# Kernel optimization log

Measured on AMD Instinct MI355X. Metric: run time of the kernel, lower is better.

Reference implementation:

```python
import jax, jax.numpy as jnp
import numpy as np

WS = 8        # window_size -> N = 64
P = 8         # patch_size
HEADS = 3
DIM = 96
B = 2048


def _relative_positions_log(ws):
    coords = jnp.stack(jnp.meshgrid(jnp.arange(ws), jnp.arange(ws), indexing='ij'))  # [2,ws,ws]
    cf = coords.reshape(2, -1)                                   # [2, N]
    rel = cf[:, :, None] - cf[:, None, :]                        # [2, N, N]
    rel = rel.transpose(1, 2, 0).astype(jnp.float32)             # [N, N, 2]
    return jnp.sign(rel) * jnp.log1p(jnp.abs(rel))


def setup_inputs() -> dict:
    key = jax.random.key(0)
    k0, k1, k2 = jax.random.split(key, 3)
    N = WS * WS
    qkv = jax.random.normal(k0, (B, N, 3 * DIM), dtype=jnp.float32)
    w1 = jax.random.normal(k1, (2, 256), dtype=jnp.float32) * 0.02
    b1 = jnp.zeros((256,), dtype=jnp.float32)
    w2 = jax.random.normal(k2, (256, HEADS), dtype=jnp.float32) * 0.02
    b2 = jnp.zeros((HEADS,), dtype=jnp.float32)
    return {"qkv": qkv, "w1": w1, "b1": b1, "w2": w2, "b2": b2}


def reference(qkv, w1, b1, w2, b2):
    B_, N, C3 = qkv.shape
    dim = C3 // 3
    h = HEADS
    d = dim // h
    scale = d ** (-0.5)

    qkv = qkv.reshape(B_, N, 3, h, d).transpose(2, 0, 3, 1, 4)   # [3,B,h,N,d]
    q, k, v = qkv[0] * scale, qkv[1], qkv[2]

    c = N // (P * P)
    def to_patch(x):  # [B,h,N,d] -> [B,h,c,d,P,P]
        return x.reshape(B_, h, c, P, P, d).transpose(0, 1, 2, 5, 3, 4)

    q_fft = jnp.fft.rfft2(to_patch(q))
    k_fft = jnp.fft.rfft2(to_patch(k))
    out = jnp.fft.irfft2(q_fft * k_fft, s=(P, P))                # [B,h,c,d,P,P]
    out = out.transpose(0, 1, 2, 4, 5, 3).reshape(B_, h, N, d)   # back to [B,h,N,d]

    rp = _relative_positions_log(WS)                             # [N,N,2]
    bias = jax.nn.relu(rp @ w1 + b1) @ w2 + b2                   # [N,N,h]
    bias = bias.transpose(2, 0, 1)                               # [h,N,N]

    attn = jnp.einsum('bhnd,bhmd->bhnm', out, v) + bias[None]
    attn = jax.nn.softmax(attn, axis=-1)
    x = jnp.einsum('bhnm,bhmd->bhnd', attn, v)
    return x.transpose(0, 2, 1, 3).reshape(B_, N, dim)
```

## Files before the change

### kernel.cpp

```cpp
#include <hip/hip_runtime.h>

#define B_TOT 2048
#define NHEAD 3

typedef __attribute__((ext_vector_type(8))) short short8v;
typedef __attribute__((ext_vector_type(4))) float f32x4;
typedef __attribute__((ext_vector_type(2))) __fp16 f16x2;

#define LOG2E 1.4426950408889634f

static __device__ __forceinline__ unsigned short f2bf(float x) {
    unsigned u = __builtin_bit_cast(unsigned, x);
    u += 0x7FFFu + ((u >> 16) & 1u);
    return (unsigned short)(u >> 16);
}
static __device__ __forceinline__ float bf2f(unsigned short s) {
    unsigned u = ((unsigned)s) << 16;
    return __builtin_bit_cast(float, u);
}
static __device__ __forceinline__ float exp2_fast(float x) {
    float r; asm("v_exp_f32 %0, %1" : "=v"(r) : "v"(x)); return r;
}

__global__ __launch_bounds__(256) void bias_kernel(const float* __restrict__ w1,
                                                   const float* __restrict__ b1,
                                                   const float* __restrict__ w2,
                                                   const float* __restrict__ b2,
                                                   float* __restrict__ bias2) {
    int t = blockIdx.x * 256 + threadIdx.x;
    int h = t >> 12;
    int lane = (t >> 6) & 63;
    int pair = t & 63;
    int g = lane >> 4, c = lane & 15;
    int mt = pair >> 4, nt = (pair >> 2) & 3, r = pair & 3;
    int n = 16 * mt + 4 * g + r;
    int m = 16 * nt + c;

    float d0 = (float)((n >> 3) - (m >> 3));
    float d1 = (float)((n & 7) - (m & 7));
    float r0 = (d0 > 0.f ? 1.f : (d0 < 0.f ? -1.f : 0.f)) * log1pf(fabsf(d0));
    float r1 = (d1 > 0.f ? 1.f : (d1 < 0.f ? -1.f : 0.f)) * log1pf(fabsf(d1));
    float a = 0.f;
    for (int j = 0; j < 256; j++) {
        float hd = fmaf(r0, w1[j], fmaf(r1, w1[256 + j], b1[j]));
        hd = fmaxf(hd, 0.f);
        a = fmaf(hd, w2[j * 3 + h], a);
    }
    bias2[((h * 16 + mt * 4 + nt) * 64 + lane) * 4 + r] = (a + b2[h]) * LOG2E;
}

__global__ __launch_bounds__(256, 3) void attn_kernel(const float* __restrict__ qkv,
                                                      const float* __restrict__ bias2,
                                                      float* __restrict__ out) {
    __shared__ float smem[4][64 * 36];

    const int t = threadIdx.x;
    const int w = t >> 6;
    const int lane = t & 63;
    const int h = blockIdx.x % 3;
    const int b = (blockIdx.x / 3) * 4 + w;

    float* Qs = smem[w];
    const float* base = qkv + (size_t)b * (64 * 288) + h * 32;
    const float QS = 0.17677669529663687f * LOG2E;

    {
        const int nr = lane >> 3, d0 = (lane & 7) * 4;
        #pragma unroll
        for (int s = 0; s < 8; s++) {
            int n = 8 * s + nr;
            float4 q4 = *(const float4*)(base + n * 288 + d0);
            q4.x *= QS; q4.y *= QS; q4.z *= QS; q4.w *= QS;
            *(float4*)(Qs + n * 36 + d0) = q4;
        }
    }

    const int dd = lane & 31, H2 = lane >> 5;
    f16x2 krp[64];
    #pragma unroll
    for (int t8 = 0; t8 < 8; t8++) {
        const int rb = ((t8 + 4 * H2) & 7) * 8;
        float k8[8];
        #pragma unroll
        for (int tx = 0; tx < 8; tx++)
            k8[tx] = base[(rb + tx) * 288 + 96 + dd];
        #pragma unroll
        for (int i = 0; i < 8; i++)
            krp[t8 * 8 + i] = __builtin_amdgcn_cvt_pkrtz(k8[i], k8[(i - 1) & 7]);
    }

    asm volatile("s_waitcnt lgkmcnt(0)" ::: "memory");

    float acc[4][8];
    #pragma unroll
    for (int yi = 0; yi < 4; yi++)
        #pragma unroll
        for (int x = 0; x < 8; x++) acc[yi][x] = 0.f;

    #pragma unroll
    for (int u = 0; u < 8; u++) {
        f16x2 q2[4];
        #pragma unroll
        for (int j = 0; j < 4; j++) {
            float qa = Qs[(u * 8 + 2 * j) * 36 + dd];
            float qb = Qs[(u * 8 + 2 * j + 1) * 36 + dd];
            q2[j] = __builtin_amdgcn_cvt_pkrtz(qa, qb);
        }
        #pragma unroll
        for (int yi = 0; yi < 4; yi++) {
            const int s = (yi - u) & 7;
            #pragma unroll
            for (int x = 0; x < 8; x++) {
                #pragma unroll
                for (int j = 0; j < 4; j++)
                    acc[yi][x] = __builtin_amdgcn_fdot2(
                        q2[j], krp[s * 8 + ((x - 2 * j) & 7)], acc[yi][x], false);
            }
        }
    }

    #pragma unroll
    for (int yi = 0; yi < 4; yi++) {
        const int n = (4 * H2 + yi) * 8;
        #pragma unroll
        for (int x = 0; x < 8; x++)
            Qs[(n + x) * 36 + dd] = acc[yi][x];
    }
    asm volatile("s_waitcnt lgkmcnt(0)" ::: "memory");

    const int g = lane >> 4, c = lane & 15;

    short8v Oh[4], Ol[4];
    #pragma unroll
    for (int mt = 0; mt < 4; mt++) {
        const float* rp = Qs + (16 * mt + c) * 36 + 8 * g;
        float4 x0 = *(const float4*)rp;
        float4 x1 = *(const float4*)(rp + 4);
        float xs[8] = {x0.x, x0.y, x0.z, x0.w, x1.x, x1.y, x1.z, x1.w};
        #pragma unroll
        for (int j = 0; j < 8; j++) {
            unsigned short hb = f2bf(xs[j]);
            Oh[mt][j] = (short)hb;
            Ol[mt][j] = (short)f2bf(xs[j] - bf2f(hb));
        }
    }

    short8v Vh[4], Vl[4];
    #pragma unroll
    for (int nt = 0; nt < 4; nt++) {
        const float* vp = base + (16 * nt + c) * 288 + 192 + 8 * g;
        float4 x0 = *(const float4*)vp;
        float4 x1 = *(const float4*)(vp + 4);
        float xs[8] = {x0.x, x0.y, x0.z, x0.w, x1.x, x1.y, x1.z, x1.w};
        #pragma unroll
        for (int j = 0; j < 8; j++) {
            unsigned short hb = f2bf(xs[j]);
            Vh[nt][j] = (short)hb;
            Vl[nt][j] = (short)f2bf(xs[j] - bf2f(hb));
        }
    }

    const float* bb = bias2 + (size_t)h * 16 * 256 + lane * 4;
    f32x4 S[4][4];
    __builtin_amdgcn_s_setprio(1);
    #pragma unroll
    for (int mt = 0; mt < 4; mt++)
        #pragma unroll
        for (int nt = 0; nt < 4; nt++) {
            f32x4 a = __builtin_bit_cast(f32x4, *(const float4*)(bb + (mt * 4 + nt) * 256));
            a = __builtin_amdgcn_mfma_f32_16x16x32_bf16(Oh[mt], Vh[nt], a, 0, 0, 0);
            a = __builtin_amdgcn_mfma_f32_16x16x32_bf16(Oh[mt], Vl[nt], a, 0, 0, 0);
            a = __builtin_amdgcn_mfma_f32_16x16x32_bf16(Ol[mt], Vh[nt], a, 0, 0, 0);
            S[mt][nt] = a;
        }
    __builtin_amdgcn_s_setprio(0);

    float vb[2][2][8];
    #pragma unroll
    for (int kt = 0; kt < 2; kt++)
        #pragma unroll
        for (int dt = 0; dt < 2; dt++)
            #pragma unroll
            for (int j = 0; j < 8; j++)
                vb[kt][dt][j] = base[(32 * kt + 8 * g + j) * 288 + 192 + 16 * dt + c];

    #pragma unroll
    for (int mt = 0; mt < 4; mt++) {
        #pragma unroll
        for (int r = 0; r < 4; r++) {
            float m0 = fmaxf(fmaxf(S[mt][0][r], S[mt][1][r]), fmaxf(S[mt][2][r], S[mt][3][r]));
            m0 = fmaxf(m0, __shfl_xor(m0, 1, 64));
            m0 = fmaxf(m0, __shfl_xor(m0, 2, 64));
            m0 = fmaxf(m0, __shfl_xor(m0, 4, 64));
            m0 = fmaxf(m0, __shfl_xor(m0, 8, 64));
            #pragma unroll
            for (int nt = 0; nt < 4; nt++)
                S[mt][nt][r] = exp2_fast(S[mt][nt][r] - m0);
        }
    }

    unsigned short* Ps = (unsigned short*)Qs;
    #pragma unroll
    for (int mt = 0; mt < 4; mt++)
        #pragma unroll
        for (int nt = 0; nt < 4; nt++)
            #pragma unroll
            for (int r = 0; r < 4; r++)
                Ps[(16 * mt + 4 * g + r) * 72 + 16 * nt + c] = f2bf(S[mt][nt][r]);
    asm volatile("s_waitcnt lgkmcnt(0)" ::: "memory");

    short8v Pf[4][2];
    #pragma unroll
    for (int mt = 0; mt < 4; mt++)
        #pragma unroll
        for (int kt = 0; kt < 2; kt++)
            Pf[mt][kt] = *(const short8v*)(Ps + (16 * mt + c) * 72 + 32 * kt + 8 * g);

    short8v Vp[2][2];
    #pragma unroll
    for (int kt = 0; kt < 2; kt++)
        #pragma unroll
        for (int dt = 0; dt < 2; dt++)
            #pragma unroll
            for (int j = 0; j < 8; j++)
                Vp[kt][dt][j] = (short)f2bf(vb[kt][dt][j]);

    short8v ones;
    #pragma unroll
    for (int j = 0; j < 8; j++) ones[j] = (short)0x3F80;
    f32x4 inv4[4];
    __builtin_amdgcn_s_setprio(1);
    #pragma unroll
    for (int mt = 0; mt < 4; mt++) {
        f32x4 sa = {0.f, 0.f, 0.f, 0.f};
        sa = __builtin_amdgcn_mfma_f32_16x16x32_bf16(Pf[mt][0], ones, sa, 0, 0, 0);
        sa = __builtin_amdgcn_mfma_f32_16x16x32_bf16(Pf[mt][1], ones, sa, 0, 0, 0);
        #pragma unroll
        for (int r = 0; r < 4; r++) inv4[mt][r] = 1.f / sa[r];
    }

    f32x4 X[4][2];
    #pragma unroll
    for (int mt = 0; mt < 4; mt++)
        #pragma unroll
        for (int dt = 0; dt < 2; dt++) {
            f32x4 a = {0.f, 0.f, 0.f, 0.f};
            a = __builtin_amdgcn_mfma_f32_16x16x32_bf16(Pf[mt][0], Vp[0][dt], a, 0, 0, 0);
            a = __builtin_amdgcn_mfma_f32_16x16x32_bf16(Pf[mt][1], Vp[1][dt], a, 0, 0, 0);
            X[mt][dt] = a;
        }
    __builtin_amdgcn_s_setprio(0);

    float* op = out + (size_t)b * (64 * 96) + h * 32;
    #pragma unroll
    for (int mt = 0; mt < 4; mt++)
        #pragma unroll
        for (int dt = 0; dt < 2; dt++)
            #pragma unroll
            for (int r = 0; r < 4; r++)
                op[(16 * mt + 4 * g + r) * 96 + 16 * dt + c] = X[mt][dt][r] * inv4[mt][r];
}

extern "C" void kernel_launch(void* const* d_in, const int* in_sizes, int n_in,
                              void* d_out, int out_size, void* d_ws, size_t ws_size,
                              hipStream_t stream) {
    const float* qkv = (const float*)d_in[0];
    const float* w1  = (const float*)d_in[1];
    const float* b1  = (const float*)d_in[2];
    const float* w2  = (const float*)d_in[3];
    const float* b2  = (const float*)d_in[4];
    float* out = (float*)d_out;
    float* bias2 = (float*)d_ws;

    bias_kernel<<<48, 256, 0, stream>>>(w1, b1, w2, b2, bias2);
    attn_kernel<<<(B_TOT / 4) * NHEAD, 256, 0, stream>>>(qkv, bias2, out);
}
```

Measured before the change: 64.95 us.

## Read Q directly from global, hoist V loads earlier, split bias MLP across lanes

The Q staging through shared memory is dropped; each lane now reads scaled Q values straight from global memory inside the FFT-convolution loop. V fragment and vb loads are moved before the MFMA phase so their latency overlaps with the conversion work, at the cost of more live registers. The bias kernel splits each 256-term reduction across 4 lanes and combines them with shuffles, launching 4x more blocks to shorten its serial loop. The risks are register pressure at occupancy 3 and repeated uncoalesced global reads of Q.

```diff
diff --git a/kernel.cpp b/kernel.cpp
--- a/kernel.cpp
+++ b/kernel.cpp
@@ -27,7 +27,8 @@
                                                    const float* __restrict__ w2,
                                                    const float* __restrict__ b2,
                                                    float* __restrict__ bias2) {
-    int t = blockIdx.x * 256 + threadIdx.x;
+    int gtid = blockIdx.x * 256 + threadIdx.x;
+    int t = gtid >> 2, sub = gtid & 3;
     int h = t >> 12;
     int lane = (t >> 6) & 63;
     int pair = t & 63;
@@ -41,12 +42,16 @@
     float r0 = (d0 > 0.f ? 1.f : (d0 < 0.f ? -1.f : 0.f)) * log1pf(fabsf(d0));
     float r1 = (d1 > 0.f ? 1.f : (d1 < 0.f ? -1.f : 0.f)) * log1pf(fabsf(d1));
     float a = 0.f;
-    for (int j = 0; j < 256; j++) {
+    for (int i = 0; i < 64; i++) {
+        int j = 4 * i + sub;
         float hd = fmaf(r0, w1[j], fmaf(r1, w1[256 + j], b1[j]));
         hd = fmaxf(hd, 0.f);
         a = fmaf(hd, w2[j * 3 + h], a);
     }
-    bias2[((h * 16 + mt * 4 + nt) * 64 + lane) * 4 + r] = (a + b2[h]) * LOG2E;
+    a += __shfl_xor(a, 1, 64);
+    a += __shfl_xor(a, 2, 64);
+    if (sub == 0)
+        bias2[((h * 16 + mt * 4 + nt) * 64 + lane) * 4 + r] = (a + b2[h]) * LOG2E;
 }
 
 __global__ __launch_bounds__(256, 3) void attn_kernel(const float* __restrict__ qkv,
@@ -63,19 +68,9 @@
     float* Qs = smem[w];
     const float* base = qkv + (size_t)b * (64 * 288) + h * 32;
     const float QS = 0.17677669529663687f * LOG2E;
-
-    {
-        const int nr = lane >> 3, d0 = (lane & 7) * 4;
-        #pragma unroll
-        for (int s = 0; s < 8; s++) {
-            int n = 8 * s + nr;
-            float4 q4 = *(const float4*)(base + n * 288 + d0);
-            q4.x *= QS; q4.y *= QS; q4.z *= QS; q4.w *= QS;
-            *(float4*)(Qs + n * 36 + d0) = q4;
-        }
-    }
-
     const int dd = lane & 31, H2 = lane >> 5;
+    const int g = lane >> 4, c = lane & 15;
+
     f16x2 krp[64];
     #pragma unroll
     for (int t8 = 0; t8 < 8; t8++) {
@@ -89,8 +84,6 @@
             krp[t8 * 8 + i] = __builtin_amdgcn_cvt_pkrtz(k8[i], k8[(i - 1) & 7]);
     }
 
-    asm volatile("s_waitcnt lgkmcnt(0)" ::: "memory");
-
     float acc[4][8];
     #pragma unroll
     for (int yi = 0; yi < 4; yi++)
@@ -102,8 +95,8 @@
         f16x2 q2[4];
         #pragma unroll
         for (int j = 0; j < 4; j++) {
-            float qa = Qs[(u * 8 + 2 * j) * 36 + dd];
-            float qb = Qs[(u * 8 + 2 * j + 1) * 36 + dd];
+            float qa = base[(u * 8 + 2 * j) * 288 + dd] * QS;
+            float qb = base[(u * 8 + 2 * j + 1) * 288 + dd] * QS;
             q2[j] = __builtin_amdgcn_cvt_pkrtz(qa, qb);
         }
         #pragma unroll
@@ -126,9 +119,24 @@
         for (int x = 0; x < 8; x++)
             Qs[(n + x) * 36 + dd] = acc[yi][x];
     }
+
+    float4 vr0[4], vr1[4];
+    #pragma unroll
+    for (int nt = 0; nt < 4; nt++) {
+        const float* vp = base + (16 * nt + c) * 288 + 192 + 8 * g;
+        vr0[nt] = *(const float4*)vp;
+        vr1[nt] = *(const float4*)(vp + 4);
+    }
+    float vb[2][2][8];
+    #pragma unroll
+    for (int kt = 0; kt < 2; kt++)
+        #pragma unroll
+        for (int dt = 0; dt < 2; dt++)
+            #pragma unroll
+            for (int j = 0; j < 8; j++)
+                vb[kt][dt][j] = base[(32 * kt + 8 * g + j) * 288 + 192 + 16 * dt + c];
+
     asm volatile("s_waitcnt lgkmcnt(0)" ::: "memory");
-
-    const int g = lane >> 4, c = lane & 15;
 
     short8v Oh[4], Ol[4];
     #pragma unroll
@@ -148,10 +156,8 @@
     short8v Vh[4], Vl[4];
     #pragma unroll
     for (int nt = 0; nt < 4; nt++) {
-        const float* vp = base + (16 * nt + c) * 288 + 192 + 8 * g;
-        float4 x0 = *(const float4*)vp;
-        float4 x1 = *(const float4*)(vp + 4);
-        float xs[8] = {x0.x, x0.y, x0.z, x0.w, x1.x, x1.y, x1.z, x1.w};
+        float xs[8] = {vr0[nt].x, vr0[nt].y, vr0[nt].z, vr0[nt].w,
+                       vr1[nt].x, vr1[nt].y, vr1[nt].z, vr1[nt].w};
         #pragma unroll
         for (int j = 0; j < 8; j++) {
             unsigned short hb = f2bf(xs[j]);
@@ -174,15 +180,6 @@
             S[mt][nt] = a;
         }
     __builtin_amdgcn_s_setprio(0);
-
-    float vb[2][2][8];
-    #pragma unroll
-    for (int kt = 0; kt < 2; kt++)
-        #pragma unroll
-        for (int dt = 0; dt < 2; dt++)
-            #pragma unroll
-            for (int j = 0; j < 8; j++)
-                vb[kt][dt][j] = base[(32 * kt + 8 * g + j) * 288 + 192 + 16 * dt + c];
 
     #pragma unroll
     for (int mt = 0; mt < 4; mt++) {
@@ -272,6 +269,6 @@
     float* out = (float*)d_out;
     float* bias2 = (float*)d_ws;
 
-    bias_kernel<<<48, 256, 0, stream>>>(w1, b1, w2, b2, bias2);
+    bias_kernel<<<192, 256, 0, stream>>>(w1, b1, w2, b2, bias2);
     attn_kernel<<<(B_TOT / 4) * NHEAD, 256, 0, stream>>>(qkv, bias2, out);
 }
```

Result: no change. 65.98 us (+1.6%).

## Process two (batch, head) units per wave and split bias reduction across lanes

Applied to the files above, without the earlier changes.

Each wave now handles two (batch, head) work units, interleaving their FFT-circulant fdot2 loops for more instruction-level parallelism, then runs the softmax/PV stage for each in turn. Shared memory doubles, launch bounds drop to 2 blocks per CU and the grid halves. Separately, the bias MLP reduction is split across 4 lanes with shuffle reduction and 4x more blocks, to shorten its serial 256-iteration loop. The doubled register footprint (two krp arrays of 64 packed halves) risks spills or lower occupancy.

```diff
diff --git a/kernel.cpp b/kernel.cpp
--- a/kernel.cpp
+++ b/kernel.cpp
@@ -27,7 +27,8 @@
                                                    const float* __restrict__ w2,
                                                    const float* __restrict__ b2,
                                                    float* __restrict__ bias2) {
-    int t = blockIdx.x * 256 + threadIdx.x;
+    int gtid = blockIdx.x * 256 + threadIdx.x;
+    int t = gtid >> 2, sub = gtid & 3;
     int h = t >> 12;
     int lane = (t >> 6) & 63;
     int pair = t & 63;
@@ -41,70 +42,87 @@
     float r0 = (d0 > 0.f ? 1.f : (d0 < 0.f ? -1.f : 0.f)) * log1pf(fabsf(d0));
     float r1 = (d1 > 0.f ? 1.f : (d1 < 0.f ? -1.f : 0.f)) * log1pf(fabsf(d1));
     float a = 0.f;
-    for (int j = 0; j < 256; j++) {
+    for (int i = 0; i < 64; i++) {
+        int j = 4 * i + sub;
         float hd = fmaf(r0, w1[j], fmaf(r1, w1[256 + j], b1[j]));
         hd = fmaxf(hd, 0.f);
         a = fmaf(hd, w2[j * 3 + h], a);
     }
-    bias2[((h * 16 + mt * 4 + nt) * 64 + lane) * 4 + r] = (a + b2[h]) * LOG2E;
-}
-
-__global__ __launch_bounds__(256, 3) void attn_kernel(const float* __restrict__ qkv,
+    a += __shfl_xor(a, 1, 64);
+    a += __shfl_xor(a, 2, 64);
+    if (sub == 0)
+        bias2[((h * 16 + mt * 4 + nt) * 64 + lane) * 4 + r] = (a + b2[h]) * LOG2E;
+}
+
+__global__ __launch_bounds__(256, 2) void attn_kernel(const float* __restrict__ qkv,
                                                       const float* __restrict__ bias2,
                                                       float* __restrict__ out) {
-    __shared__ float smem[4][64 * 36];
+    __shared__ float smem[8][64 * 36];
 
     const int t = threadIdx.x;
     const int w = t >> 6;
     const int lane = t & 63;
-    const int h = blockIdx.x % 3;
-    const int b = (blockIdx.x / 3) * 4 + w;
-
-    float* Qs = smem[w];
-    const float* base = qkv + (size_t)b * (64 * 288) + h * 32;
+    const int u0 = (blockIdx.x * 4 + w) * 2;
+    const int u1 = u0 + 1;
+    const int b0 = u0 / 3, h0 = u0 % 3;
+    const int b1 = u1 / 3, h1 = u1 % 3;
+
+    float* QsA = smem[w * 2];
+    float* QsB = smem[w * 2 + 1];
+    const float* baseA = qkv + (size_t)b0 * (64 * 288) + h0 * 32;
+    const float* baseB = qkv + (size_t)b1 * (64 * 288) + h1 * 32;
     const float QS = 0.17677669529663687f * LOG2E;
+    const int dd = lane & 31, H2 = lane >> 5;
+    const int g = lane >> 4, c = lane & 15;
 
     {
         const int nr = lane >> 3, d0 = (lane & 7) * 4;
         #pragma unroll
         for (int s = 0; s < 8; s++) {
             int n = 8 * s + nr;
-            float4 q4 = *(const float4*)(base + n * 288 + d0);
-            q4.x *= QS; q4.y *= QS; q4.z *= QS; q4.w *= QS;
-            *(float4*)(Qs + n * 36 + d0) = q4;
-        }
-    }
-
-    const int dd = lane & 31, H2 = lane >> 5;
-    f16x2 krp[64];
+            float4 qa = *(const float4*)(baseA + n * 288 + d0);
+            float4 qb = *(const float4*)(baseB + n * 288 + d0);
+            qa.x *= QS; qa.y *= QS; qa.z *= QS; qa.w *= QS;
+            qb.x *= QS; qb.y *= QS; qb.z *= QS; qb.w *= QS;
+            *(float4*)(QsA + n * 36 + d0) = qa;
+            *(float4*)(QsB + n * 36 + d0) = qb;
+        }
+    }
+
+    f16x2 krpA[64], krpB[64];
     #pragma unroll
     for (int t8 = 0; t8 < 8; t8++) {
         const int rb = ((t8 + 4 * H2) & 7) * 8;
-        float k8[8];
-        #pragma unroll
-        for (int tx = 0; tx < 8; tx++)
-            k8[tx] = base[(rb + tx) * 288 + 96 + dd];
-        #pragma unroll
-        for (int i = 0; i < 8; i++)
-            krp[t8 * 8 + i] = __builtin_amdgcn_cvt_pkrtz(k8[i], k8[(i - 1) & 7]);
+        float kA[8], kB[8];
+        #pragma unroll
+        for (int tx = 0; tx < 8; tx++) {
+            kA[tx] = baseA[(rb + tx) * 288 + 96 + dd];
+            kB[tx] = baseB[(rb + tx) * 288 + 96 + dd];
+        }
+        #pragma unroll
+        for (int i = 0; i < 8; i++) {
+            krpA[t8 * 8 + i] = __builtin_amdgcn_cvt_pkrtz(kA[i], kA[(i - 1) & 7]);
+            krpB[t8 * 8 + i] = __builtin_amdgcn_cvt_pkrtz(kB[i], kB[(i - 1) & 7]);
+        }
     }
 
     asm volatile("s_waitcnt lgkmcnt(0)" ::: "memory");
 
-    float acc[4][8];
+    float accA[4][8], accB[4][8];
     #pragma unroll
     for (int yi = 0; yi < 4; yi++)
         #pragma unroll
-        for (int x = 0; x < 8; x++) acc[yi][x] = 0.f;
+        for (int x = 0; x < 8; x++) { accA[yi][x] = 0.f; accB[yi][x] = 0.f; }
 
     #pragma unroll
     for (int u = 0; u < 8; u++) {
-        f16x2 q2[4];
+        f16x2 q2A[4], q2B[4];
         #pragma unroll
         for (int j = 0; j < 4; j++) {
-            float qa = Qs[(u * 8 + 2 * j) * 36 + dd];
-            float qb = Qs[(u * 8 + 2 * j + 1) * 36 + dd];
-            q2[j] = __builtin_amdgcn_cvt_pkrtz(qa, qb);
+            q2A[j] = __builtin_amdgcn_cvt_pkrtz(QsA[(u * 8 + 2 * j) * 36 + dd],
+                                                QsA[(u * 8 + 2 * j + 1) * 36 + dd]);
+            q2B[j] = __builtin_amdgcn_cvt_pkrtz(QsB[(u * 8 + 2 * j) * 36 + dd],
+                                                QsB[(u * 8 + 2 * j + 1) * 36 + dd]);
         }
         #pragma unroll
         for (int yi = 0; yi < 4; yi++) {
@@ -112,9 +130,12 @@
             #pragma unroll
             for (int x = 0; x < 8; x++) {
                 #pragma unroll
-                for (int j = 0; j < 4; j++)
-                    acc[yi][x] = __builtin_amdgcn_fdot2(
-                        q2[j], krp[s * 8 + ((x - 2 * j) & 7)], acc[yi][x], false);
+                for (int j = 0; j < 4; j++) {
+                    accA[yi][x] = __builtin_amdgcn_fdot2(
+                        q2A[j], krpA[s * 8 + ((x - 2 * j) & 7)], accA[yi][x], false);
+                    accB[yi][x] = __builtin_amdgcn_fdot2(
+                        q2B[j], krpB[s * 8 + ((x - 2 * j) & 7)], accB[yi][x], false);
+                }
             }
         }
     }
@@ -123,142 +144,148 @@
     for (int yi = 0; yi < 4; yi++) {
         const int n = (4 * H2 + yi) * 8;
         #pragma unroll
-        for (int x = 0; x < 8; x++)
-            Qs[(n + x) * 36 + dd] = acc[yi][x];
+        for (int x = 0; x < 8; x++) {
+            QsA[(n + x) * 36 + dd] = accA[yi][x];
+            QsB[(n + x) * 36 + dd] = accB[yi][x];
+        }
     }
     asm volatile("s_waitcnt lgkmcnt(0)" ::: "memory");
 
-    const int g = lane >> 4, c = lane & 15;
-
-    short8v Oh[4], Ol[4];
-    #pragma unroll
-    for (int mt = 0; mt < 4; mt++) {
-        const float* rp = Qs + (16 * mt + c) * 36 + 8 * g;
-        float4 x0 = *(const float4*)rp;
-        float4 x1 = *(const float4*)(rp + 4);
-        float xs[8] = {x0.x, x0.y, x0.z, x0.w, x1.x, x1.y, x1.z, x1.w};
-        #pragma unroll
-        for (int j = 0; j < 8; j++) {
-            unsigned short hb = f2bf(xs[j]);
-            Oh[mt][j] = (short)hb;
-            Ol[mt][j] = (short)f2bf(xs[j] - bf2f(hb));
-        }
-    }
-
-    short8v Vh[4], Vl[4];
-    #pragma unroll
-    for (int nt = 0; nt < 4; nt++) {
-        const float* vp = base + (16 * nt + c) * 288 + 192 + 8 * g;
-        float4 x0 = *(const float4*)vp;
-        float4 x1 = *(const float4*)(vp + 4);
-        float xs[8] = {x0.x, x0.y, x0.z, x0.w, x1.x, x1.y, x1.z, x1.w};
-        #pragma unroll
-        for (int j = 0; j < 8; j++) {
-            unsigned short hb = f2bf(xs[j]);
-            Vh[nt][j] = (short)hb;
-            Vl[nt][j] = (short)f2bf(xs[j] - bf2f(hb));
-        }
-    }
-
-    const float* bb = bias2 + (size_t)h * 16 * 256 + lane * 4;
-    f32x4 S[4][4];
-    __builtin_amdgcn_s_setprio(1);
-    #pragma unroll
-    for (int mt = 0; mt < 4; mt++)
+    auto back_half = [&](const float* base, float* Qs, int h, int b) {
+        short8v Oh[4], Ol[4];
+        #pragma unroll
+        for (int mt = 0; mt < 4; mt++) {
+            const float* rp = Qs + (16 * mt + c) * 36 + 8 * g;
+            float4 x0 = *(const float4*)rp;
+            float4 x1 = *(const float4*)(rp + 4);
+            float xs[8] = {x0.x, x0.y, x0.z, x0.w, x1.x, x1.y, x1.z, x1.w};
+            #pragma unroll
+            for (int j = 0; j < 8; j++) {
+                unsigned short hb = f2bf(xs[j]);
+                Oh[mt][j] = (short)hb;
+                Ol[mt][j] = (short)f2bf(xs[j] - bf2f(hb));
+            }
+        }
+
+        short8v Vh[4], Vl[4];
         #pragma unroll
         for (int nt = 0; nt < 4; nt++) {
-            f32x4 a = __builtin_bit_cast(f32x4, *(const float4*)(bb + (mt * 4 + nt) * 256));
-            a = __builtin_amdgcn_mfma_f32_16x16x32_bf16(Oh[mt], Vh[nt], a, 0, 0, 0);
-            a = __builtin_amdgcn_mfma_f32_16x16x32_bf16(Oh[mt], Vl[nt], a, 0, 0, 0);
-            a = __builtin_amdgcn_mfma_f32_16x16x32_bf16(Ol[mt], Vh[nt], a, 0, 0, 0);
-            S[mt][nt] = a;
-        }
-    __builtin_amdgcn_s_setprio(0);
-
-    float vb[2][2][8];
-    #pragma unroll
-    for (int kt = 0; kt < 2; kt++)
-        #pragma unroll
-        for (int dt = 0; dt < 2; dt++)
-            #pragma unroll
-            for (int j = 0; j < 8; j++)
-                vb[kt][dt][j] = base[(32 * kt + 8 * g + j) * 288 + 192 + 16 * dt + c];
-
-    #pragma unroll
-    for (int mt = 0; mt < 4; mt++) {
-        #pragma unroll
-        for (int r = 0; r < 4; r++) {
-            float m0 = fmaxf(fmaxf(S[mt][0][r], S[mt][1][r]), fmaxf(S[mt][2][r], S[mt][3][r]));
-            m0 = fmaxf(m0, __shfl_xor(m0, 1, 64));
-            m0 = fmaxf(m0, __shfl_xor(m0, 2, 64));
-            m0 = fmaxf(m0, __shfl_xor(m0, 4, 64));
-            m0 = fmaxf(m0, __shfl_xor(m0, 8, 64));
+            const float* vp = base + (16 * nt + c) * 288 + 192 + 8 * g;
+            float4 x0 = *(const float4*)vp;
+            float4 x1 = *(const float4*)(vp + 4);
+            float xs[8] = {x0.x, x0.y, x0.z, x0.w, x1.x, x1.y, x1.z, x1.w};
+            #pragma unroll
+            for (int j = 0; j < 8; j++) {
+                unsigned short hb = f2bf(xs[j]);
+                Vh[nt][j] = (short)hb;
+                Vl[nt][j] = (short)f2bf(xs[j] - bf2f(hb));
+            }
+        }
+
+        const float* bb = bias2 + (size_t)h * 16 * 256 + lane * 4;
+        f32x4 S[4][4];
+        __builtin_amdgcn_s_setprio(1);
+        #pragma unroll
+        for (int mt = 0; mt < 4; mt++)
+            #pragma unroll
+            for (int nt = 0; nt < 4; nt++) {
+                f32x4 a = __builtin_bit_cast(f32x4, *(const float4*)(bb + (mt * 4 + nt) * 256));
+                a = __builtin_amdgcn_mfma_f32_16x16x32_bf16(Oh[mt], Vh[nt], a, 0, 0, 0);
+                a = __builtin_amdgcn_mfma_f32_16x16x32_bf16(Oh[mt], Vl[nt], a, 0, 0, 0);
+                a = __builtin_amdgcn_mfma_f32_16x16x32_bf16(Ol[mt], Vh[nt], a, 0, 0, 0);
+                S[mt][nt] = a;
+            }
+        __builtin_amdgcn_s_setprio(0);
+
+        float vb[2][2][8];
+        #pragma unroll
+        for (int kt = 0; kt < 2; kt++)
+            #pragma unroll
+            for (int dt = 0; dt < 2; dt++)
+                #pragma unroll
+                for (int j = 0; j < 8; j++)
+                    vb[kt][dt][j] = base[(32 * kt + 8 * g + j) * 288 + 192 + 16 * dt + c];
+
+        #pragma unroll
+        for (int mt = 0; mt < 4; mt++) {
+            #pragma unroll
+            for (int r = 0; r < 4; r++) {
+                float m0 = fmaxf(fmaxf(S[mt][0][r], S[mt][1][r]),
+                                 fmaxf(S[mt][2][r], S[mt][3][r]));
+                m0 = fmaxf(m0, __shfl_xor(m0, 1, 64));
+                m0 = fmaxf(m0, __shfl_xor(m0, 2, 64));
+                m0 = fmaxf(m0, __shfl_xor(m0, 4, 64));
+                m0 = fmaxf(m0, __shfl_xor(m0, 8, 64));
+                #pragma unroll
+                for (int nt = 0; nt < 4; nt++)
+                    S[mt][nt][r] = exp2_fast(S[mt][nt][r] - m0);
+            }
+        }
+
+        unsigned short* Ps = (unsigned short*)Qs;
+        #pragma unroll
+        for (int mt = 0; mt < 4; mt++)
             #pragma unroll
             for (int nt = 0; nt < 4; nt++)
-                S[mt][nt][r] = exp2_fast(S[mt][nt][r] - m0);
-        }
-    }
-
-    unsigned short* Ps = (unsigned short*)Qs;
-    #pragma unroll
-    for (int mt = 0; mt < 4; mt++)
-        #pragma unroll
-        for (int nt = 0; nt < 4; nt++)
-            #pragma unroll
-            for (int r = 0; r < 4; r++)
-                Ps[(16 * mt + 4 * g + r) * 72 + 16 * nt + c] = f2bf(S[mt][nt][r]);
-    asm volatile("s_waitcnt lgkmcnt(0)" ::: "memory");
-
-    short8v Pf[4][2];
-    #pragma unroll
-    for (int mt = 0; mt < 4; mt++)
+                #pragma unroll
+                for (int r = 0; r < 4; r++)
+                    Ps[(16 * mt + 4 * g + r) * 72 + 16 * nt + c] = f2bf(S[mt][nt][r]);
+        asm volatile("s_waitcnt lgkmcnt(0)" ::: "memory");
+
+        short8v Pf[4][2];
+        #pragma unroll
+        for (int mt = 0; mt < 4; mt++)
+            #pragma unroll
+            for (int kt = 0; kt < 2; kt++)
+                Pf[mt][kt] = *(const short8v*)(Ps + (16 * mt + c) * 72 + 32 * kt + 8 * g);
+
+        short8v Vp[2][2];
         #pragma unroll
         for (int kt = 0; kt < 2; kt++)
-            Pf[mt][kt] = *(const short8v*)(Ps + (16 * mt + c) * 72 + 32 * kt + 8 * g);
-
-    short8v Vp[2][2];
-    #pragma unroll
-    for (int kt = 0; kt < 2; kt++)
-        #pragma unroll
-        for (int dt = 0; dt < 2; dt++)
-            #pragma unroll
-            for (int j = 0; j < 8; j++)
-                Vp[kt][dt][j] = (short)f2bf(vb[kt][dt][j]);
-
-    short8v ones;
-    #pragma unroll
-    for (int j = 0; j < 8; j++) ones[j] = (short)0x3F80;
-    f32x4 inv4[4];
-    __builtin_amdgcn_s_setprio(1);
-    #pragma unroll
-    for (int mt = 0; mt < 4; mt++) {
-        f32x4 sa = {0.f, 0.f, 0.f, 0.f};
-        sa = __builtin_amdgcn_mfma_f32_16x16x32_bf16(Pf[mt][0], ones, sa, 0, 0, 0);
-        sa = __builtin_amdgcn_mfma_f32_16x16x32_bf16(Pf[mt][1], ones, sa, 0, 0, 0);
-        #pragma unroll
-        for (int r = 0; r < 4; r++) inv4[mt][r] = 1.f / sa[r];
-    }
-
-    f32x4 X[4][2];
-    #pragma unroll
-    for (int mt = 0; mt < 4; mt++)
-        #pragma unroll
-        for (int dt = 0; dt < 2; dt++) {
-            f32x4 a = {0.f, 0.f, 0.f, 0.f};
-            a = __builtin_amdgcn_mfma_f32_16x16x32_bf16(Pf[mt][0], Vp[0][dt], a, 0, 0, 0);
-            a = __builtin_amdgcn_mfma_f32_16x16x32_bf16(Pf[mt][1], Vp[1][dt], a, 0, 0, 0);
-            X[mt][dt] = a;
-        }
-    __builtin_amdgcn_s_setprio(0);
-
-    float* op = out + (size_t)b * (64 * 96) + h * 32;
-    #pragma unroll
-    for (int mt = 0; mt < 4; mt++)
-        #pragma unroll
-        for (int dt = 0; dt < 2; dt++)
-            #pragma unroll
-            for (int r = 0; r < 4; r++)
-                op[(16 * mt + 4 * g + r) * 96 + 16 * dt + c] = X[mt][dt][r] * inv4[mt][r];
+            #pragma unroll
+            for (int dt = 0; dt < 2; dt++)
+                #pragma unroll
+                for (int j = 0; j < 8; j++)
+                    Vp[kt][dt][j] = (short)f2bf(vb[kt][dt][j]);
+
+        short8v ones;
+        #pragma unroll
+        for (int j = 0; j < 8; j++) ones[j] = (short)0x3F80;
+        f32x4 inv4[4];
+        __builtin_amdgcn_s_setprio(1);
+        #pragma unroll
+        for (int mt = 0; mt < 4; mt++) {
+            f32x4 sa = {0.f, 0.f, 0.f, 0.f};
+            sa = __builtin_amdgcn_mfma_f32_16x16x32_bf16(Pf[mt][0], ones, sa, 0, 0, 0);
+            sa = __builtin_amdgcn_mfma_f32_16x16x32_bf16(Pf[mt][1], ones, sa, 0, 0, 0);
+            #pragma unroll
+            for (int r = 0; r < 4; r++) inv4[mt][r] = 1.f / sa[r];
+        }
+
+        f32x4 X[4][2];
+        #pragma unroll
+        for (int mt = 0; mt < 4; mt++)
+            #pragma unroll
+            for (int dt = 0; dt < 2; dt++) {
+                f32x4 a = {0.f, 0.f, 0.f, 0.f};
+                a = __builtin_amdgcn_mfma_f32_16x16x32_bf16(Pf[mt][0], Vp[0][dt], a, 0, 0, 0);
+                a = __builtin_amdgcn_mfma_f32_16x16x32_bf16(Pf[mt][1], Vp[1][dt], a, 0, 0, 0);
+                X[mt][dt] = a;
+            }
+        __builtin_amdgcn_s_setprio(0);
+
+        float* op = out + (size_t)b * (64 * 96) + h * 32;
+        #pragma unroll
+        for (int mt = 0; mt < 4; mt++)
+            #pragma unroll
+            for (int dt = 0; dt < 2; dt++)
+                #pragma unroll
+                for (int r = 0; r < 4; r++)
+                    op[(16 * mt + 4 * g + r) * 96 + 16 * dt + c] = X[mt][dt][r] * inv4[mt][r];
+    };
+
+    back_half(baseA, QsA, h0, b0);
+    back_half(baseB, QsB, h1, b1);
 }
 
 extern "C" void kernel_launch(void* const* d_in, const int* in_sizes, int n_in,
@@ -272,6 +299,6 @@
     float* out = (float*)d_out;
     float* bias2 = (float*)d_ws;
 
-    bias_kernel<<<48, 256, 0, stream>>>(w1, b1, w2, b2, bias2);
-    attn_kernel<<<(B_TOT / 4) * NHEAD, 256, 0, stream>>>(qkv, bias2, out);
-}
+    bias_kernel<<<192, 256, 0, stream>>>(w1, b1, w2, b2, bias2);
+    attn_kernel<<<(B_TOT * NHEAD) / 8, 256, 0, stream>>>(qkv, bias2, out);
+}
```

After: 77.03 us. 18.6% more time.

## Stage K via global_load_lds, prefetch Q early, split bias reduction across lanes

Applied to the files above, without the earlier changes.

K tiles are now loaded straight into LDS with global_load_lds in a coalesced pattern and read back per column, replacing strided scalar global loads. Q loads are issued up front into registers so they overlap with the K loads, and are scaled and stored to LDS afterwards. The bias kernel splits its 256-term reduction across 4 lanes with shuffle reductions and launches four times as many blocks. The attention kernel's launch bounds drop the minimum blocks per CU from 3 to 2, which allows more registers per thread but may lower occupancy.

```diff
diff --git a/kernel.cpp b/kernel.cpp
--- a/kernel.cpp
+++ b/kernel.cpp
@@ -6,6 +6,9 @@
 typedef __attribute__((ext_vector_type(8))) short short8v;
 typedef __attribute__((ext_vector_type(4))) float f32x4;
 typedef __attribute__((ext_vector_type(2))) __fp16 f16x2;
+
+typedef __attribute__((address_space(1))) const void* gas_ptr;
+typedef __attribute__((address_space(3))) void* las_ptr;
 
 #define LOG2E 1.4426950408889634f
 
@@ -27,7 +30,8 @@
                                                    const float* __restrict__ w2,
                                                    const float* __restrict__ b2,
                                                    float* __restrict__ bias2) {
-    int t = blockIdx.x * 256 + threadIdx.x;
+    int gtid = blockIdx.x * 256 + threadIdx.x;
+    int t = gtid >> 2, sub = gtid & 3;
     int h = t >> 12;
     int lane = (t >> 6) & 63;
     int pair = t & 63;
@@ -41,15 +45,19 @@
     float r0 = (d0 > 0.f ? 1.f : (d0 < 0.f ? -1.f : 0.f)) * log1pf(fabsf(d0));
     float r1 = (d1 > 0.f ? 1.f : (d1 < 0.f ? -1.f : 0.f)) * log1pf(fabsf(d1));
     float a = 0.f;
-    for (int j = 0; j < 256; j++) {
+    for (int i = 0; i < 64; i++) {
+        int j = 4 * i + sub;
         float hd = fmaf(r0, w1[j], fmaf(r1, w1[256 + j], b1[j]));
         hd = fmaxf(hd, 0.f);
         a = fmaf(hd, w2[j * 3 + h], a);
     }
-    bias2[((h * 16 + mt * 4 + nt) * 64 + lane) * 4 + r] = (a + b2[h]) * LOG2E;
-}
-
-__global__ __launch_bounds__(256, 3) void attn_kernel(const float* __restrict__ qkv,
+    a += __shfl_xor(a, 1, 64);
+    a += __shfl_xor(a, 2, 64);
+    if (sub == 0)
+        bias2[((h * 16 + mt * 4 + nt) * 64 + lane) * 4 + r] = (a + b2[h]) * LOG2E;
+}
+
+__global__ __launch_bounds__(256, 2) void attn_kernel(const float* __restrict__ qkv,
                                                       const float* __restrict__ bias2,
                                                       float* __restrict__ out) {
     __shared__ float smem[4][64 * 36];
@@ -63,19 +71,24 @@
     float* Qs = smem[w];
     const float* base = qkv + (size_t)b * (64 * 288) + h * 32;
     const float QS = 0.17677669529663687f * LOG2E;
-
-    {
-        const int nr = lane >> 3, d0 = (lane & 7) * 4;
-        #pragma unroll
-        for (int s = 0; s < 8; s++) {
-            int n = 8 * s + nr;
-            float4 q4 = *(const float4*)(base + n * 288 + d0);
-            q4.x *= QS; q4.y *= QS; q4.z *= QS; q4.w *= QS;
-            *(float4*)(Qs + n * 36 + d0) = q4;
-        }
-    }
-
     const int dd = lane & 31, H2 = lane >> 5;
+    const int g = lane >> 4, c = lane & 15;
+    const int nr = lane >> 3, d0q = (lane & 7) * 4;
+
+    #pragma unroll
+    for (int s = 0; s < 8; s++) {
+        const float* gsrc = base + (8 * s + nr) * 288 + 96 + d0q;
+        __builtin_amdgcn_global_load_lds((gas_ptr)gsrc, (las_ptr)(Qs + s * 256),
+                                         16, 0, 0);
+    }
+
+    float4 qreg[8];
+    #pragma unroll
+    for (int s = 0; s < 8; s++)
+        qreg[s] = *(const float4*)(base + (8 * s + nr) * 288 + d0q);
+
+    asm volatile("s_waitcnt vmcnt(0)" ::: "memory");
+
     f16x2 krp[64];
     #pragma unroll
     for (int t8 = 0; t8 < 8; t8++) {
@@ -83,12 +96,19 @@
         float k8[8];
         #pragma unroll
         for (int tx = 0; tx < 8; tx++)
-            k8[tx] = base[(rb + tx) * 288 + 96 + dd];
+            k8[tx] = Qs[(rb + tx) * 32 + dd];
         #pragma unroll
         for (int i = 0; i < 8; i++)
             krp[t8 * 8 + i] = __builtin_amdgcn_cvt_pkrtz(k8[i], k8[(i - 1) & 7]);
     }
-
+    __builtin_amdgcn_sched_barrier(0);
+
+    #pragma unroll
+    for (int s = 0; s < 8; s++) {
+        float4 q4 = qreg[s];
+        q4.x *= QS; q4.y *= QS; q4.z *= QS; q4.w *= QS;
+        *(float4*)(Qs + (8 * s + nr) * 36 + d0q) = q4;
+    }
     asm volatile("s_waitcnt lgkmcnt(0)" ::: "memory");
 
     float acc[4][8];
@@ -127,8 +147,6 @@
             Qs[(n + x) * 36 + dd] = acc[yi][x];
     }
     asm volatile("s_waitcnt lgkmcnt(0)" ::: "memory");
-
-    const int g = lane >> 4, c = lane & 15;
 
     short8v Oh[4], Ol[4];
     #pragma unroll
@@ -272,6 +290,6 @@
     float* out = (float*)d_out;
     float* bias2 = (float*)d_ws;
 
-    bias_kernel<<<48, 256, 0, stream>>>(w1, b1, w2, b2, bias2);
+    bias_kernel<<<192, 256, 0, stream>>>(w1, b1, w2, b2, bias2);
     attn_kernel<<<(B_TOT / 4) * NHEAD, 256, 0, stream>>>(qkv, bias2, out);
 }
```

Result: faster. 60.58 us (-6.7%).
